# Performance work log

Measured on AMD Instinct MI355X. Metric: run time of the kernel, lower is better.

The kernel has to match this reference:

```python
import jax, jax.numpy as jnp
import numpy as np

B, L, D, H = 2, 2048, 1024, 16
HD = D // H
SCALE = HD ** -0.5


def setup_inputs() -> dict:
    key = jax.random.key(0)
    ks = jax.random.split(key, 11)
    s = D ** -0.5  # torch Linear default init scale (uniform bound)
    return {
        "q": jax.random.normal(ks[0], (B, L, D), jnp.float32),
        "k": jax.random.normal(ks[1], (B, L, D), jnp.float32),
        "v": jax.random.normal(ks[2], (B, L, D), jnp.float32),
        "Wq": jax.random.uniform(ks[3], (D, D), jnp.float32, -s, s),
        "bq": jax.random.uniform(ks[4], (D,), jnp.float32, -s, s),
        "Wk": jax.random.uniform(ks[5], (D, D), jnp.float32, -s, s),
        "bk": jax.random.uniform(ks[6], (D,), jnp.float32, -s, s),
        "Wv": jax.random.uniform(ks[7], (D, D), jnp.float32, -s, s),
        "bv": jax.random.uniform(ks[8], (D,), jnp.float32, -s, s),
        "Wo": jax.random.uniform(ks[9], (D, D), jnp.float32, -s, s),
        "bo": jax.random.uniform(ks[10], (D,), jnp.float32, -s, s),
    }


def reference(q, k, v, Wq, bq, Wk, bk, Wv, bv, Wo, bo):
    b, q_len, _ = q.shape
    # projections; weights stored as (D, D) acting on the right: x @ W + b
    qh = (q @ Wq + bq).reshape(b, q_len, H, HD).transpose(0, 2, 1, 3)  # (B,H,Q,hd)
    kh = (k @ Wk + bk).reshape(b, -1, H, HD).transpose(0, 2, 1, 3)    # (B,H,K,hd)
    vh = (v @ Wv + bv).reshape(b, -1, H, HD).transpose(0, 2, 1, 3)    # (B,H,K,hd)
    att = jnp.einsum("bhqd,bhkd->bhqk", qh * SCALE, kh)               # (B,H,Q,K)
    att = jax.nn.softmax(att, axis=-1)
    out = jnp.einsum("bhqk,bhkd->bhqd", att, vh)                      # (B,H,Q,hd)
    out = out.transpose(0, 2, 1, 3).reshape(b, q_len, D)
    return out @ Wo + bo
```

## Files before the change

kernel.cpp:

```cpp
#include <hip/hip_runtime.h>

namespace {
constexpr int kB  = 2;
constexpr int kL  = 2048;
constexpr int kD  = 1024;
constexpr int kH  = 16;
constexpr int kHD = 64;
constexpr int kM  = kB * kL;
}

typedef _Float16 f16x8 __attribute__((ext_vector_type(8)));
typedef float    f32x16 __attribute__((ext_vector_type(16)));
typedef unsigned int u32;

union Frag16 { uint4 u4; unsigned u[4]; f16x8 v; };

__device__ __forceinline__ unsigned short f2h(float f) {
    return __builtin_bit_cast(unsigned short, (_Float16)f);
}
__device__ __forceinline__ unsigned pk2(float a, float b) {
    return __builtin_bit_cast(unsigned, __builtin_amdgcn_cvt_pkrtz(a, b));
}
__device__ __forceinline__ float max3f(float a, float b, float c) {
    float d;
    asm("v_max3_f32 %0, %1, %2, %3" : "=v"(d) : "v"(a), "v"(b), "v"(c));
    return d;
}

__device__ __forceinline__ void gload16(const void* g, void* l) {
    __builtin_amdgcn_global_load_lds(
        (const __attribute__((address_space(1))) u32*)g,
        (__attribute__((address_space(3))) u32*)(unsigned long long)(__builtin_bit_cast(unsigned long long, l)),
        16, 0, 0);
}

__global__ __launch_bounds__(256) void cast_f16_kernel(
    const float* __restrict__ q, const float* __restrict__ k,
    const float* __restrict__ v, unsigned short* __restrict__ dst)
{
    const float* src = blockIdx.y == 0 ? q : (blockIdx.y == 1 ? k : v);
    unsigned short* d = dst + (size_t)blockIdx.y * ((size_t)kM * kD);
    const size_t i = ((size_t)blockIdx.x * 256 + threadIdx.x) * 8;
    const float4 f0 = *(const float4*)(src + i);
    const float4 f1 = *(const float4*)(src + i + 4);
    _Float16 h[8];
    h[0] = (_Float16)f0.x; h[1] = (_Float16)f0.y;
    h[2] = (_Float16)f0.z; h[3] = (_Float16)f0.w;
    h[4] = (_Float16)f1.x; h[5] = (_Float16)f1.y;
    h[6] = (_Float16)f1.z; h[7] = (_Float16)f1.w;
    *(uint4*)(d + i) = *(uint4*)h;
}

__global__ __launch_bounds__(256) void tcast_kernel(
    const float* __restrict__ W0, const float* __restrict__ W1,
    const float* __restrict__ W2, const float* __restrict__ W3,
    unsigned short* __restrict__ WtBase)
{
    __shared__ _Float16 T[64][68];
    const float* W = blockIdx.z == 0 ? W0 : blockIdx.z == 1 ? W1
                   : blockIdx.z == 2 ? W2 : W3;
    unsigned short* Wt = WtBase + (size_t)blockIdx.z * ((size_t)kD * kD);
    const int k0 = blockIdx.y * 64, n0 = blockIdx.x * 64;
    const int tx = threadIdx.x & 15, ty = threadIdx.x >> 4;
#pragma unroll
    for (int i = 0; i < 4; ++i) {
        const int kk = i * 16 + ty;
        const float4 w = *(const float4*)&W[(size_t)(k0 + kk) * kD + n0 + tx * 4];
        T[tx * 4 + 0][kk] = (_Float16)w.x;
        T[tx * 4 + 1][kk] = (_Float16)w.y;
        T[tx * 4 + 2][kk] = (_Float16)w.z;
        T[tx * 4 + 3][kk] = (_Float16)w.w;
    }
    __syncthreads();
#pragma unroll
    for (int i = 0; i < 4; ++i) {
        const int nn = i * 16 + ty;
        *(ushort4*)&Wt[(size_t)(n0 + nn) * kD + k0 + tx * 4] = *(ushort4*)&T[nn][tx * 4];
    }
}

template <int MODE>
__global__ __launch_bounds__(256) void gemm16_kernel(
    const unsigned short* __restrict__ A, const unsigned short* __restrict__ Wt,
    const float* __restrict__ bias, void* __restrict__ Cv)
{
    __shared__ unsigned short Als[3][128 * 64];
    __shared__ unsigned short Bls[3][128 * 64];

    const int tid = threadIdx.x;
    const int lane = tid & 63;
    const int wid = tid >> 6;
    const int l31 = lane & 31;
    const int hi = lane >> 5;
    const int by = blockIdx.x & 31;
    const int bx = blockIdx.x >> 5;
    const int row0 = by * 128;
    const int col0 = bx * 128;
    const int wr = wid >> 1, wc = wid & 1;

    const int rl = lane >> 3;
    const int sl = lane & 7;
    const int ssrc = (sl ^ rl) * 8;

    const unsigned short* Abase = A + (size_t)(row0 + wid * 32 + rl) * kD + ssrc;
    const unsigned short* Bbase = Wt + (size_t)(col0 + wid * 32 + rl) * kD + ssrc;

    f32x16 acc00{}, acc01{}, acc10{}, acc11{};

    auto stage = [&](int kt, int buf) {
#pragma unroll
        for (int i = 0; i < 4; ++i) {
            gload16(Abase + (size_t)(i * 8) * kD + kt * 64,
                    &Als[buf][(wid * 32 + i * 8) * 64]);
        }
#pragma unroll
        for (int i = 0; i < 4; ++i) {
            gload16(Bbase + (size_t)(i * 8) * kD + kt * 64,
                    &Bls[buf][(wid * 32 + i * 8) * 64]);
        }
    };

    const int ra0 = wr * 64 + l31;
    const int cb0 = wc * 64 + l31;

    stage(0, 0);
    stage(1, 1);
    int cur = 0, stg = 2;
    for (int kt = 0; kt < kD / 64; ++kt) {
        if (kt < kD / 64 - 1) asm volatile("s_waitcnt vmcnt(8)" ::: "memory");
        else                  asm volatile("s_waitcnt vmcnt(0)" ::: "memory");
        __builtin_amdgcn_s_barrier();
        if (kt + 2 < kD / 64) {
            stage(kt + 2, stg);
            stg = (stg + 1 == 3) ? 0 : stg + 1;
        }
#pragma unroll
        for (int ks = 0; ks < 4; ++ks) {
            const int slot = (ks << 1) | hi;
            Frag16 a0, a1, b0, b1;
            a0.u4 = *(const uint4*)&Als[cur][ra0 * 64 + ((slot ^ (ra0 & 7)) << 3)];
            a1.u4 = *(const uint4*)&Als[cur][(ra0 + 32) * 64 + ((slot ^ ((ra0 + 32) & 7)) << 3)];
            b0.u4 = *(const uint4*)&Bls[cur][cb0 * 64 + ((slot ^ (cb0 & 7)) << 3)];
            b1.u4 = *(const uint4*)&Bls[cur][(cb0 + 32) * 64 + ((slot ^ ((cb0 + 32) & 7)) << 3)];
            acc00 = __builtin_amdgcn_mfma_f32_32x32x16_f16(a0.v, b0.v, acc00, 0, 0, 0);
            acc01 = __builtin_amdgcn_mfma_f32_32x32x16_f16(a0.v, b1.v, acc01, 0, 0, 0);
            acc10 = __builtin_amdgcn_mfma_f32_32x32x16_f16(a1.v, b0.v, acc10, 0, 0, 0);
            acc11 = __builtin_amdgcn_mfma_f32_32x32x16_f16(a1.v, b1.v, acc11, 0, 0, 0);
        }
        cur = (cur + 1 == 3) ? 0 : cur + 1;
    }

    const float bias0 = bias[col0 + wc * 64 + l31];
    const float bias1 = bias[col0 + wc * 64 + 32 + l31];

    const f32x16* accs[2][2] = {{&acc00, &acc01}, {&acc10, &acc11}};
#pragma unroll
    for (int rt = 0; rt < 2; ++rt) {
#pragma unroll
        for (int ct = 0; ct < 2; ++ct) {
            const f32x16& acv = *accs[rt][ct];
            const float bb = ct ? bias1 : bias0;
            const int c = col0 + wc * 64 + ct * 32 + l31;
            if (MODE == 2) {
                unsigned short* C = (unsigned short*)Cv;
#pragma unroll
                for (int qd = 0; qd < 4; ++qd) {
                    const int r = row0 + wr * 64 + rt * 32 + 8 * qd + 4 * hi;
                    const int b_ = r >> 11, l_ = r & (kL - 1);
                    ushort4 w;
                    w.x = f2h(acv[4 * qd + 0] + bb);
                    w.y = f2h(acv[4 * qd + 1] + bb);
                    w.z = f2h(acv[4 * qd + 2] + bb);
                    w.w = f2h(acv[4 * qd + 3] + bb);
                    *(ushort4*)&C[((size_t)(b_ * kH + (c >> 6)) * kHD + (c & 63)) * kL + l_] = w;
                }
            } else {
#pragma unroll
                for (int reg = 0; reg < 16; ++reg) {
                    const int r = row0 + wr * 64 + rt * 32 + (reg & 3) + 8 * (reg >> 2) + 4 * hi;
                    const float val = acv[reg] + bb;
                    if (MODE == 0) {
                        ((float*)Cv)[(size_t)r * kD + c] = val;
                    } else {
                        const int b_ = r >> 11, l_ = r & (kL - 1);
                        ((unsigned short*)Cv)[((size_t)(b_ * kH + (c >> 6)) * kL + l_) * kHD + (c & 63)] = f2h(val);
                    }
                }
            }
        }
    }
}

__global__ __launch_bounds__(512) void attn_mfma_kernel(
    const unsigned short* __restrict__ Qh, const unsigned short* __restrict__ Kh,
    const unsigned short* __restrict__ Vt, unsigned short* __restrict__ Opart,
    float2* __restrict__ Stat)
{
    __shared__ unsigned short Kls[4][64 * 64];
    __shared__ unsigned short Vls[4][64 * 64];

    const int lane = threadIdx.x & 63;
    const int wid  = threadIdx.x >> 6;
    const int l31  = lane & 31;
    const int hi   = lane >> 5;

    const int id = blockIdx.x;
    const int j  = id >> 3;
    const int bh = (id & 7) * 4 + (j >> 4);
    const int qt = j & 7;
    const int ks = (j >> 3) & 1;
    const int q = qt * 256 + wid * 32 + l31;

    const size_t qkBase = (size_t)bh * kL * kHD;
    const unsigned short* Qp = Qh + qkBase + (size_t)q * kHD + hi * 8;
    Frag16 qf[4];
#pragma unroll
    for (int d = 0; d < 4; ++d) qf[d].u4 = *(const uint4*)(Qp + d * 16);

    const int srow = wid * 8 + (lane >> 3);
    const int soff = (((lane & 7) ^ (srow & 7)) << 3);
    const unsigned short* Kg = Kh + qkBase + (size_t)srow * kHD + soff;
    const unsigned short* Vg = Vt + (size_t)bh * kHD * kL + (size_t)srow * kL + soff;

    auto stage = [&](int kt, int buf) {
        gload16(Kg + (size_t)(kt * 64) * kHD, &Kls[buf][(wid * 8) * 64]);
        gload16(Vg + kt * 64,                 &Vls[buf][(wid * 8) * 64]);
    };

    f16x8 onesv;
#pragma unroll
    for (int i = 0; i < 8; ++i) onesv[i] = (_Float16)1.0f;

    f32x16 o0{}, o1{}, ls{};
    float m = -1e30f;
    const float cexp = 0.125f * 1.44269504089f;

    auto process = [&](int cur) {
        const int rA = l31, rB = l31 + 32;
        f32x16 c0{}, c1{};
        Frag16 kf0[4], kf1[4];
#pragma unroll
        for (int d = 0; d < 4; ++d) {
            const int s = (d << 1) | hi;
            kf0[d].u4 = *(const uint4*)&Kls[cur][rA * 64 + ((s ^ (rA & 7)) << 3)];
            kf1[d].u4 = *(const uint4*)&Kls[cur][rB * 64 + ((s ^ (rB & 7)) << 3)];
        }
        Frag16 vf0[4], vf1[4];
#pragma unroll
        for (int ksl = 0; ksl < 4; ++ksl) {
            const int s = (ksl << 1) | hi;
            vf0[ksl].u4 = *(const uint4*)&Vls[cur][rA * 64 + ((s ^ (rA & 7)) << 3)];
            vf1[ksl].u4 = *(const uint4*)&Vls[cur][rB * 64 + ((s ^ (rB & 7)) << 3)];
        }
        __builtin_amdgcn_s_setprio(1);
#pragma unroll
        for (int d = 0; d < 4; ++d) {
            c0 = __builtin_amdgcn_mfma_f32_32x32x16_f16(kf0[d].v, qf[d].v, c0, 0, 0, 0);
            c1 = __builtin_amdgcn_mfma_f32_32x32x16_f16(kf1[d].v, qf[d].v, c1, 0, 0, 0);
        }
        __builtin_amdgcn_s_setprio(0);

        float mx = fmaxf(c0[0], c1[0]);
#pragma unroll
        for (int r = 1; r < 16; ++r) mx = max3f(mx, c0[r], c1[r]);
        mx = fmaxf(mx, __shfl_xor(mx, 32));
        if (mx > m + 48.f) {
            const float corr = __builtin_amdgcn_exp2f((m - mx) * cexp);
            m = mx;
            o0 *= corr;
            o1 *= corr;
            ls *= corr;
        }
        const float mc = m * cexp;

        unsigned u0[8], u1[8];
#pragma unroll
        for (int i = 0; i < 8; ++i) {
            u0[i] = pk2(__builtin_amdgcn_exp2f(fmaf(c0[2 * i], cexp, -mc)),
                        __builtin_amdgcn_exp2f(fmaf(c0[2 * i + 1], cexp, -mc)));
            u1[i] = pk2(__builtin_amdgcn_exp2f(fmaf(c1[2 * i], cexp, -mc)),
                        __builtin_amdgcn_exp2f(fmaf(c1[2 * i + 1], cexp, -mc)));
        }
        Frag16 pf[4];
        {
            unsigned t0 = hi ? u0[0] : u0[2];
            unsigned t1 = hi ? u0[1] : u0[3];
            unsigned t2 = hi ? u0[4] : u0[6];
            unsigned t3 = hi ? u0[5] : u0[7];
            const unsigned r0 = __shfl_xor(t0, 32);
            const unsigned r1 = __shfl_xor(t1, 32);
            const unsigned r2 = __shfl_xor(t2, 32);
            const unsigned r3 = __shfl_xor(t3, 32);
            pf[0].u[0] = hi ? r0 : u0[0];
            pf[0].u[1] = hi ? r1 : u0[1];
            pf[0].u[2] = hi ? u0[2] : r0;
            pf[0].u[3] = hi ? u0[3] : r1;
            pf[1].u[0] = hi ? r2 : u0[4];
            pf[1].u[1] = hi ? r3 : u0[5];
            pf[1].u[2] = hi ? u0[6] : r2;
            pf[1].u[3] = hi ? u0[7] : r3;
        }
        {
            unsigned t0 = hi ? u1[0] : u1[2];
            unsigned t1 = hi ? u1[1] : u1[3];
            unsigned t2 = hi ? u1[4] : u1[6];
            unsigned t3 = hi ? u1[5] : u1[7];
            const unsigned r0 = __shfl_xor(t0, 32);
            const unsigned r1 = __shfl_xor(t1, 32);
            const unsigned r2 = __shfl_xor(t2, 32);
            const unsigned r3 = __shfl_xor(t3, 32);
            pf[2].u[0] = hi ? r0 : u1[0];
            pf[2].u[1] = hi ? r1 : u1[1];
            pf[2].u[2] = hi ? u1[2] : r0;
            pf[2].u[3] = hi ? u1[3] : r1;
            pf[3].u[0] = hi ? r2 : u1[4];
            pf[3].u[1] = hi ? r3 : u1[5];
            pf[3].u[2] = hi ? u1[6] : r2;
            pf[3].u[3] = hi ? u1[7] : r3;
        }

        __builtin_amdgcn_s_setprio(1);
#pragma unroll
        for (int ksl = 0; ksl < 4; ++ksl) {
            o0 = __builtin_amdgcn_mfma_f32_32x32x16_f16(vf0[ksl].v, pf[ksl].v, o0, 0, 0, 0);
            o1 = __builtin_amdgcn_mfma_f32_32x32x16_f16(vf1[ksl].v, pf[ksl].v, o1, 0, 0, 0);
            ls = __builtin_amdgcn_mfma_f32_32x32x16_f16(onesv, pf[ksl].v, ls, 0, 0, 0);
        }
        __builtin_amdgcn_s_setprio(0);
    };

    const int kt0 = ks * 16;
    stage(kt0 + 0, 0);
    stage(kt0 + 1, 1);

    for (int rt = 0; rt < 8; ++rt) {
        const int t0 = 2 * rt;
        asm volatile("s_waitcnt vmcnt(0)" ::: "memory");
        __builtin_amdgcn_s_barrier();
        if (t0 + 3 < 16) {
            stage(kt0 + t0 + 2, (t0 + 2) & 3);
            stage(kt0 + t0 + 3, (t0 + 3) & 3);
        }
        process(t0 & 3);
        process((t0 + 1) & 3);
    }

    const float lsum = ls[0];
    const size_t prow = (size_t)ks * (32 * kL) + (size_t)bh * kL + q;
    const float inv = 1.f / lsum;
    unsigned short* pp = Opart + prow * kHD;
#pragma unroll
    for (int g = 0; g < 4; ++g) {
        const int d = g * 8 + hi * 4;
        uint2 w0, w1;
        w0.x = pk2(o0[4 * g + 0] * inv, o0[4 * g + 1] * inv);
        w0.y = pk2(o0[4 * g + 2] * inv, o0[4 * g + 3] * inv);
        w1.x = pk2(o1[4 * g + 0] * inv, o1[4 * g + 1] * inv);
        w1.y = pk2(o1[4 * g + 2] * inv, o1[4 * g + 3] * inv);
        *(uint2*)(pp + d) = w0;
        *(uint2*)(pp + 32 + d) = w1;
    }
    if (hi == 0) Stat[prow] = make_float2(m, lsum);
}

__global__ __launch_bounds__(256) void merge_kernel(
    const unsigned short* __restrict__ Opart, const float2* __restrict__ Stat,
    unsigned short* __restrict__ O16)
{
    const int g = blockIdx.x * 256 + threadIdx.x;
    const int row = g >> 3;
    const int d0 = (g & 7) * 8;
    const int bh = row >> 11, q = row & (kL - 1);
    const float2 sa = Stat[row];
    const float2 sb = Stat[32 * kL + row];
    const float cexp = 0.125f * 1.44269504089f;
    const float M = fmaxf(sa.x, sb.x);
    float wa = __builtin_amdgcn_exp2f((sa.x - M) * cexp) * sa.y;
    float wb = __builtin_amdgcn_exp2f((sb.x - M) * cexp) * sb.y;
    const float inv = 1.f / (wa + wb);
    wa *= inv; wb *= inv;

    const unsigned short* pa = Opart + (size_t)row * kHD + d0;
    const unsigned short* pb = pa + (size_t)32 * kL * kHD;
    uint4 ua = *(const uint4*)pa;
    uint4 ub = *(const uint4*)pb;
    _Float16 ha[8], hb[8];
    *(uint4*)ha = ua;
    *(uint4*)hb = ub;
    unsigned out[4];
#pragma unroll
    for (int i = 0; i < 4; ++i) {
        const float v0 = wa * (float)ha[2 * i]     + wb * (float)hb[2 * i];
        const float v1 = wa * (float)ha[2 * i + 1] + wb * (float)hb[2 * i + 1];
        out[i] = pk2(v0, v1);
    }
    const int b_ = bh >> 4, h_ = bh & 15;
    *(uint4*)&O16[((size_t)(b_ * kL + q)) * kD + h_ * kHD + d0] = *(uint4*)out;
}

extern "C" void kernel_launch(void* const* d_in, const int* in_sizes, int n_in,
                              void* d_out, int out_size, void* d_ws, size_t ws_size,
                              hipStream_t stream)
{
    const float* q  = (const float*)d_in[0];
    const float* k  = (const float*)d_in[1];
    const float* v  = (const float*)d_in[2];
    const float* Wq = (const float*)d_in[3];
    const float* bq = (const float*)d_in[4];
    const float* Wk = (const float*)d_in[5];
    const float* bk = (const float*)d_in[6];
    const float* Wv = (const float*)d_in[7];
    const float* bv = (const float*)d_in[8];
    const float* Wo = (const float*)d_in[9];
    const float* bo = (const float*)d_in[10];
    float* out = (float*)d_out;

    const size_t MD = (size_t)kM * kD;
    const size_t DD = (size_t)kD * kD;
    unsigned short* A16 = (unsigned short*)d_ws;
    unsigned short* Wt16 = A16 + 3 * MD;
    unsigned short* Qh16 = Wt16 + 4 * DD;
    unsigned short* Kh16 = Qh16 + MD;
    unsigned short* Vt16 = Kh16 + MD;
    unsigned short* O16   = A16;
    unsigned short* Opart = A16 + MD;
    float2*         Stat  = (float2*)Wt16;

    const dim3 blk(256);

    hipLaunchKernelGGL(cast_f16_kernel, dim3(kM * kD / (256 * 8), 3), blk, 0, stream,
                       q, k, v, A16);
    hipLaunchKernelGGL(tcast_kernel, dim3(16, 16, 4), blk, 0, stream,
                       Wq, Wk, Wv, Wo, Wt16);

    hipLaunchKernelGGL((gemm16_kernel<1>), dim3(256), blk, 0, stream,
                       A16, Wt16, bq, (void*)Qh16);
    hipLaunchKernelGGL((gemm16_kernel<1>), dim3(256), blk, 0, stream,
                       A16 + MD, Wt16 + DD, bk, (void*)Kh16);
    hipLaunchKernelGGL((gemm16_kernel<2>), dim3(256), blk, 0, stream,
                       A16 + 2 * MD, Wt16 + 2 * DD, bv, (void*)Vt16);

    hipLaunchKernelGGL(attn_mfma_kernel, dim3(512), dim3(512), 0, stream,
                       Qh16, Kh16, Vt16, Opart, Stat);
    hipLaunchKernelGGL(merge_kernel, dim3(2048), blk, 0, stream,
                       Opart, Stat, O16);

    hipLaunchKernelGGL((gemm16_kernel<0>), dim3(256), blk, 0, stream,
                       O16, Wt16 + 3 * DD, bo, (void*)out);
}
```

Before: 136.6 us.

## Halve GEMM K-tile and merge two attention tiles per softmax step

The projection GEMM now stages 32-wide K slices instead of 64, with a 4-way XOR swizzle, 32 iterations and a matching vmcnt wait, which shrinks LDS use and may raise occupancy. The attention kernel now computes scores for two 64-key tiles together, does one max/rescale per pair, and sums the row totals with VALU adds instead of an extra ones-vector MFMA. K/V fragments are loaded from LDS inline next to their MFMAs rather than preloaded. The tradeoffs are more loop iterations and barriers in the GEMM and more live registers in attention.

```diff
diff --git a/kernel.cpp b/kernel.cpp
--- a/kernel.cpp
+++ b/kernel.cpp
@@ -84,8 +84,8 @@
     const unsigned short* __restrict__ A, const unsigned short* __restrict__ Wt,
     const float* __restrict__ bias, void* __restrict__ Cv)
 {
-    __shared__ unsigned short Als[3][128 * 64];
-    __shared__ unsigned short Bls[3][128 * 64];
+    __shared__ unsigned short Als[3][128 * 32];
+    __shared__ unsigned short Bls[3][128 * 32];
 
     const int tid = threadIdx.x;
     const int lane = tid & 63;
@@ -98,26 +98,20 @@
     const int col0 = bx * 128;
     const int wr = wid >> 1, wc = wid & 1;
 
-    const int rl = lane >> 3;
-    const int sl = lane & 7;
-    const int ssrc = (sl ^ rl) * 8;
-
-    const unsigned short* Abase = A + (size_t)(row0 + wid * 32 + rl) * kD + ssrc;
-    const unsigned short* Bbase = Wt + (size_t)(col0 + wid * 32 + rl) * kD + ssrc;
+    const int srow = wid * 16 + (lane >> 2);
+    const int ssl  = lane & 3;
+    const int ssrc = (ssl ^ ((srow >> 1) & 3)) * 8;
+
+    const unsigned short* Abase = A + (size_t)(row0 + srow) * kD + ssrc;
+    const unsigned short* Bbase = Wt + (size_t)(col0 + srow) * kD + ssrc;
 
     f32x16 acc00{}, acc01{}, acc10{}, acc11{};
 
     auto stage = [&](int kt, int buf) {
-#pragma unroll
-        for (int i = 0; i < 4; ++i) {
-            gload16(Abase + (size_t)(i * 8) * kD + kt * 64,
-                    &Als[buf][(wid * 32 + i * 8) * 64]);
-        }
-#pragma unroll
-        for (int i = 0; i < 4; ++i) {
-            gload16(Bbase + (size_t)(i * 8) * kD + kt * 64,
-                    &Bls[buf][(wid * 32 + i * 8) * 64]);
-        }
+        gload16(Abase + kt * 32,                   &Als[buf][(wid * 16) * 32]);
+        gload16(Abase + (size_t)64 * kD + kt * 32, &Als[buf][(wid * 16 + 64) * 32]);
+        gload16(Bbase + kt * 32,                   &Bls[buf][(wid * 16) * 32]);
+        gload16(Bbase + (size_t)64 * kD + kt * 32, &Bls[buf][(wid * 16 + 64) * 32]);
     };
 
     const int ra0 = wr * 64 + l31;
@@ -126,22 +120,22 @@
     stage(0, 0);
     stage(1, 1);
     int cur = 0, stg = 2;
-    for (int kt = 0; kt < kD / 64; ++kt) {
-        if (kt < kD / 64 - 1) asm volatile("s_waitcnt vmcnt(8)" ::: "memory");
-        else                  asm volatile("s_waitcnt vmcnt(0)" ::: "memory");
+    for (int kt = 0; kt < 32; ++kt) {
+        if (kt < 31) asm volatile("s_waitcnt vmcnt(4)" ::: "memory");
+        else         asm volatile("s_waitcnt vmcnt(0)" ::: "memory");
         __builtin_amdgcn_s_barrier();
-        if (kt + 2 < kD / 64) {
+        if (kt + 2 < 32) {
             stage(kt + 2, stg);
             stg = (stg + 1 == 3) ? 0 : stg + 1;
         }
 #pragma unroll
-        for (int ks = 0; ks < 4; ++ks) {
+        for (int ks = 0; ks < 2; ++ks) {
             const int slot = (ks << 1) | hi;
             Frag16 a0, a1, b0, b1;
-            a0.u4 = *(const uint4*)&Als[cur][ra0 * 64 + ((slot ^ (ra0 & 7)) << 3)];
-            a1.u4 = *(const uint4*)&Als[cur][(ra0 + 32) * 64 + ((slot ^ ((ra0 + 32) & 7)) << 3)];
-            b0.u4 = *(const uint4*)&Bls[cur][cb0 * 64 + ((slot ^ (cb0 & 7)) << 3)];
-            b1.u4 = *(const uint4*)&Bls[cur][(cb0 + 32) * 64 + ((slot ^ ((cb0 + 32) & 7)) << 3)];
+            a0.u4 = *(const uint4*)&Als[cur][ra0 * 32 + ((slot ^ ((ra0 >> 1) & 3)) << 3)];
+            a1.u4 = *(const uint4*)&Als[cur][(ra0 + 32) * 32 + ((slot ^ (((ra0 + 32) >> 1) & 3)) << 3)];
+            b0.u4 = *(const uint4*)&Bls[cur][cb0 * 32 + ((slot ^ ((cb0 >> 1) & 3)) << 3)];
+            b1.u4 = *(const uint4*)&Bls[cur][(cb0 + 32) * 32 + ((slot ^ (((cb0 + 32) >> 1) & 3)) << 3)];
             acc00 = __builtin_amdgcn_mfma_f32_32x32x16_f16(a0.v, b0.v, acc00, 0, 0, 0);
             acc01 = __builtin_amdgcn_mfma_f32_32x32x16_f16(a0.v, b1.v, acc01, 0, 0, 0);
             acc10 = __builtin_amdgcn_mfma_f32_32x32x16_f16(a1.v, b0.v, acc10, 0, 0, 0);
@@ -227,107 +221,29 @@
         gload16(Vg + kt * 64,                 &Vls[buf][(wid * 8) * 64]);
     };
 
-    f16x8 onesv;
-#pragma unroll
-    for (int i = 0; i < 8; ++i) onesv[i] = (_Float16)1.0f;
-
-    f32x16 o0{}, o1{}, ls{};
-    float m = -1e30f;
+    auto buildpf = [&](const unsigned* u, Frag16* pf) {
+        unsigned t0 = hi ? u[0] : u[2];
+        unsigned t1 = hi ? u[1] : u[3];
+        unsigned t2 = hi ? u[4] : u[6];
+        unsigned t3 = hi ? u[5] : u[7];
+        const unsigned r0 = __shfl_xor(t0, 32);
+        const unsigned r1 = __shfl_xor(t1, 32);
+        const unsigned r2 = __shfl_xor(t2, 32);
+        const unsigned r3 = __shfl_xor(t3, 32);
+        pf[0].u[0] = hi ? r0 : u[0];
+        pf[0].u[1] = hi ? r1 : u[1];
+        pf[0].u[2] = hi ? u[2] : r0;
+        pf[0].u[3] = hi ? u[3] : r1;
+        pf[1].u[0] = hi ? r2 : u[4];
+        pf[1].u[1] = hi ? r3 : u[5];
+        pf[1].u[2] = hi ? u[6] : r2;
+        pf[1].u[3] = hi ? u[7] : r3;
+    };
+
+    f32x16 o0{}, o1{};
+    float m = -1e30f, lsum = 0.f;
     const float cexp = 0.125f * 1.44269504089f;
-
-    auto process = [&](int cur) {
-        const int rA = l31, rB = l31 + 32;
-        f32x16 c0{}, c1{};
-        Frag16 kf0[4], kf1[4];
-#pragma unroll
-        for (int d = 0; d < 4; ++d) {
-            const int s = (d << 1) | hi;
-            kf0[d].u4 = *(const uint4*)&Kls[cur][rA * 64 + ((s ^ (rA & 7)) << 3)];
-            kf1[d].u4 = *(const uint4*)&Kls[cur][rB * 64 + ((s ^ (rB & 7)) << 3)];
-        }
-        Frag16 vf0[4], vf1[4];
-#pragma unroll
-        for (int ksl = 0; ksl < 4; ++ksl) {
-            const int s = (ksl << 1) | hi;
-            vf0[ksl].u4 = *(const uint4*)&Vls[cur][rA * 64 + ((s ^ (rA & 7)) << 3)];
-            vf1[ksl].u4 = *(const uint4*)&Vls[cur][rB * 64 + ((s ^ (rB & 7)) << 3)];
-        }
-        __builtin_amdgcn_s_setprio(1);
-#pragma unroll
-        for (int d = 0; d < 4; ++d) {
-            c0 = __builtin_amdgcn_mfma_f32_32x32x16_f16(kf0[d].v, qf[d].v, c0, 0, 0, 0);
-            c1 = __builtin_amdgcn_mfma_f32_32x32x16_f16(kf1[d].v, qf[d].v, c1, 0, 0, 0);
-        }
-        __builtin_amdgcn_s_setprio(0);
-
-        float mx = fmaxf(c0[0], c1[0]);
-#pragma unroll
-        for (int r = 1; r < 16; ++r) mx = max3f(mx, c0[r], c1[r]);
-        mx = fmaxf(mx, __shfl_xor(mx, 32));
-        if (mx > m + 48.f) {
-            const float corr = __builtin_amdgcn_exp2f((m - mx) * cexp);
-            m = mx;
-            o0 *= corr;
-            o1 *= corr;
-            ls *= corr;
-        }
-        const float mc = m * cexp;
-
-        unsigned u0[8], u1[8];
-#pragma unroll
-        for (int i = 0; i < 8; ++i) {
-            u0[i] = pk2(__builtin_amdgcn_exp2f(fmaf(c0[2 * i], cexp, -mc)),
-                        __builtin_amdgcn_exp2f(fmaf(c0[2 * i + 1], cexp, -mc)));
-            u1[i] = pk2(__builtin_amdgcn_exp2f(fmaf(c1[2 * i], cexp, -mc)),
-                        __builtin_amdgcn_exp2f(fmaf(c1[2 * i + 1], cexp, -mc)));
-        }
-        Frag16 pf[4];
-        {
-            unsigned t0 = hi ? u0[0] : u0[2];
-            unsigned t1 = hi ? u0[1] : u0[3];
-            unsigned t2 = hi ? u0[4] : u0[6];
-            unsigned t3 = hi ? u0[5] : u0[7];
-            const unsigned r0 = __shfl_xor(t0, 32);
-            const unsigned r1 = __shfl_xor(t1, 32);
-            const unsigned r2 = __shfl_xor(t2, 32);
-            const unsigned r3 = __shfl_xor(t3, 32);
-            pf[0].u[0] = hi ? r0 : u0[0];
-            pf[0].u[1] = hi ? r1 : u0[1];
-            pf[0].u[2] = hi ? u0[2] : r0;
-            pf[0].u[3] = hi ? u0[3] : r1;
-            pf[1].u[0] = hi ? r2 : u0[4];
-            pf[1].u[1] = hi ? r3 : u0[5];
-            pf[1].u[2] = hi ? u0[6] : r2;
-            pf[1].u[3] = hi ? u0[7] : r3;
-        }
-        {
-            unsigned t0 = hi ? u1[0] : u1[2];
-            unsigned t1 = hi ? u1[1] : u1[3];
-            unsigned t2 = hi ? u1[4] : u1[6];
-            unsigned t3 = hi ? u1[5] : u1[7];
-            const unsigned r0 = __shfl_xor(t0, 32);
-            const unsigned r1 = __shfl_xor(t1, 32);
-            const unsigned r2 = __shfl_xor(t2, 32);
-            const unsigned r3 = __shfl_xor(t3, 32);
-            pf[2].u[0] = hi ? r0 : u1[0];
-            pf[2].u[1] = hi ? r1 : u1[1];
-            pf[2].u[2] = hi ? u1[2] : r0;
-            pf[2].u[3] = hi ? u1[3] : r1;
-            pf[3].u[0] = hi ? r2 : u1[4];
-            pf[3].u[1] = hi ? r3 : u1[5];
-            pf[3].u[2] = hi ? u1[6] : r2;
-            pf[3].u[3] = hi ? u1[7] : r3;
-        }
-
-        __builtin_amdgcn_s_setprio(1);
-#pragma unroll
-        for (int ksl = 0; ksl < 4; ++ksl) {
-            o0 = __builtin_amdgcn_mfma_f32_32x32x16_f16(vf0[ksl].v, pf[ksl].v, o0, 0, 0, 0);
-            o1 = __builtin_amdgcn_mfma_f32_32x32x16_f16(vf1[ksl].v, pf[ksl].v, o1, 0, 0, 0);
-            ls = __builtin_amdgcn_mfma_f32_32x32x16_f16(onesv, pf[ksl].v, ls, 0, 0, 0);
-        }
-        __builtin_amdgcn_s_setprio(0);
-    };
+    const int rA = l31, rB = l31 + 32;
 
     const int kt0 = ks * 16;
     stage(kt0 + 0, 0);
@@ -341,11 +257,96 @@
             stage(kt0 + t0 + 2, (t0 + 2) & 3);
             stage(kt0 + t0 + 3, (t0 + 3) & 3);
         }
-        process(t0 & 3);
-        process((t0 + 1) & 3);
-    }
-
-    const float lsum = ls[0];
+        const int bA = t0 & 3, bB = (t0 + 1) & 3;
+
+        f32x16 c0{}, c1{}, c2{}, c3{};
+        __builtin_amdgcn_s_setprio(1);
+#pragma unroll
+        for (int d = 0; d < 4; ++d) {
+            const int s = (d << 1) | hi;
+            Frag16 ka0, ka1, kb0, kb1;
+            ka0.u4 = *(const uint4*)&Kls[bA][rA * 64 + ((s ^ (rA & 7)) << 3)];
+            ka1.u4 = *(const uint4*)&Kls[bA][rB * 64 + ((s ^ (rB & 7)) << 3)];
+            kb0.u4 = *(const uint4*)&Kls[bB][rA * 64 + ((s ^ (rA & 7)) << 3)];
+            kb1.u4 = *(const uint4*)&Kls[bB][rB * 64 + ((s ^ (rB & 7)) << 3)];
+            c0 = __builtin_amdgcn_mfma_f32_32x32x16_f16(ka0.v, qf[d].v, c0, 0, 0, 0);
+            c1 = __builtin_amdgcn_mfma_f32_32x32x16_f16(ka1.v, qf[d].v, c1, 0, 0, 0);
+            c2 = __builtin_amdgcn_mfma_f32_32x32x16_f16(kb0.v, qf[d].v, c2, 0, 0, 0);
+            c3 = __builtin_amdgcn_mfma_f32_32x32x16_f16(kb1.v, qf[d].v, c3, 0, 0, 0);
+        }
+        __builtin_amdgcn_s_setprio(0);
+
+        float mx = fmaxf(fmaxf(c0[0], c1[0]), fmaxf(c2[0], c3[0]));
+#pragma unroll
+        for (int r = 1; r < 16; ++r) {
+            mx = max3f(mx, c0[r], c1[r]);
+            mx = max3f(mx, c2[r], c3[r]);
+        }
+        mx = fmaxf(mx, __shfl_xor(mx, 32));
+        if (mx > m + 48.f) {
+            const float corr = __builtin_amdgcn_exp2f((m - mx) * cexp);
+            m = mx;
+            lsum *= corr;
+            o0 *= corr;
+            o1 *= corr;
+        }
+        const float mc = m * cexp;
+
+        float rs = 0.f;
+        unsigned uA0[8], uA1[8], uB0[8], uB1[8];
+#pragma unroll
+        for (int i = 0; i < 8; ++i) {
+            const float e0 = __builtin_amdgcn_exp2f(fmaf(c0[2 * i], cexp, -mc));
+            const float e1 = __builtin_amdgcn_exp2f(fmaf(c0[2 * i + 1], cexp, -mc));
+            const float e2 = __builtin_amdgcn_exp2f(fmaf(c1[2 * i], cexp, -mc));
+            const float e3 = __builtin_amdgcn_exp2f(fmaf(c1[2 * i + 1], cexp, -mc));
+            const float e4 = __builtin_amdgcn_exp2f(fmaf(c2[2 * i], cexp, -mc));
+            const float e5 = __builtin_amdgcn_exp2f(fmaf(c2[2 * i + 1], cexp, -mc));
+            const float e6 = __builtin_amdgcn_exp2f(fmaf(c3[2 * i], cexp, -mc));
+            const float e7 = __builtin_amdgcn_exp2f(fmaf(c3[2 * i + 1], cexp, -mc));
+            uA0[i] = pk2(e0, e1);
+            uA1[i] = pk2(e2, e3);
+            uB0[i] = pk2(e4, e5);
+            uB1[i] = pk2(e6, e7);
+            rs += ((e0 + e1) + (e2 + e3)) + ((e4 + e5) + (e6 + e7));
+        }
+        rs += __shfl_xor(rs, 32);
+        lsum += rs;
+
+        {
+            Frag16 pf[4];
+            buildpf(uA0, &pf[0]);
+            buildpf(uA1, &pf[2]);
+            __builtin_amdgcn_s_setprio(1);
+#pragma unroll
+            for (int ksl = 0; ksl < 4; ++ksl) {
+                const int s = (ksl << 1) | hi;
+                Frag16 v0, v1;
+                v0.u4 = *(const uint4*)&Vls[bA][rA * 64 + ((s ^ (rA & 7)) << 3)];
+                v1.u4 = *(const uint4*)&Vls[bA][rB * 64 + ((s ^ (rB & 7)) << 3)];
+                o0 = __builtin_amdgcn_mfma_f32_32x32x16_f16(v0.v, pf[ksl].v, o0, 0, 0, 0);
+                o1 = __builtin_amdgcn_mfma_f32_32x32x16_f16(v1.v, pf[ksl].v, o1, 0, 0, 0);
+            }
+            __builtin_amdgcn_s_setprio(0);
+        }
+        {
+            Frag16 pf[4];
+            buildpf(uB0, &pf[0]);
+            buildpf(uB1, &pf[2]);
+            __builtin_amdgcn_s_setprio(1);
+#pragma unroll
+            for (int ksl = 0; ksl < 4; ++ksl) {
+                const int s = (ksl << 1) | hi;
+                Frag16 v0, v1;
+                v0.u4 = *(const uint4*)&Vls[bB][rA * 64 + ((s ^ (rA & 7)) << 3)];
+                v1.u4 = *(const uint4*)&Vls[bB][rB * 64 + ((s ^ (rB & 7)) << 3)];
+                o0 = __builtin_amdgcn_mfma_f32_32x32x16_f16(v0.v, pf[ksl].v, o0, 0, 0, 0);
+                o1 = __builtin_amdgcn_mfma_f32_32x32x16_f16(v1.v, pf[ksl].v, o1, 0, 0, 0);
+            }
+            __builtin_amdgcn_s_setprio(0);
+        }
+    }
+
     const size_t prow = (size_t)ks * (32 * kL) + (size_t)bh * kL + q;
     const float inv = 1.f / lsum;
     unsigned short* pp = Opart + prow * kHD;
```

New measurement: 139.8 us. 2.3% more time.
